# Kernel tuning notes

Hardware: AMD Instinct MI355X
Metric: run time of the kernel (lower is better)

The kernel has to match this reference:

```python
import jax, jax.numpy as jnp
import numpy as np

B, M, N, R, FIN, D, H = 16, 512, 512, 8, 4, 256, 4
DH = D // H
LGAT = 2
TF_RATE, THRESH = 0.9, 2.0
GAT_W, ORG_W, DET_W = 0.5, 0.5, 0.5


def setup_inputs() -> dict:
    key = jax.random.key(0)
    ks = jax.random.split(key, 16)
    g = lambda k, shp, fan: jax.random.normal(k, shp, jnp.float32) / np.sqrt(fan)
    inp = {
        'tracks': jax.random.normal(ks[0], (B, M, R, FIN), jnp.float32),
        'detections': jax.random.normal(ks[1], (B, N, FIN), jnp.float32),
        'tracklet_marks': jax.random.randint(ks[2], (B,), M // 2, M + 1, jnp.int32),
        'detection_marks': jax.random.randint(ks[3], (B,), N // 2, N + 1, jnp.int32),
        'feat_W1': g(ks[4], (FIN, D), FIN),
        'feat_b1': jnp.zeros((D,), jnp.float32),
        'feat_W2': g(ks[5], (D, D), D),
        'feat_b2': jnp.zeros((D,), jnp.float32),
        'enc_Wqkv': g(ks[6], (D, 3 * D), D),
        'enc_Wo': g(ks[7], (D, D), D),
        'enc_ff1': g(ks[8], (D, 4 * D), D),
        'enc_ff2': g(ks[9], (4 * D, D), 4 * D),
        'gat_W': g(ks[10], (LGAT, D, D), D),
        'gat_a': g(ks[11], (LGAT, 2, H, DH), DH),
        'det_gat_W': g(ks[12], (LGAT, D, D), D),
        'det_gat_a': g(ks[13], (LGAT, 2, H, DH), DH),
        'cls_Wq': g(ks[14], (2, D, D), D),
        'cls_Wk': g(ks[15], (2, D, D), D),
    }
    return inp


def _ln(x):
    m = jnp.mean(x, -1, keepdims=True)
    v = jnp.var(x, -1, keepdims=True)
    return (x - m) * jax.lax.rsqrt(v + 1e-5)


def _feat(x, W1, b1, W2, b2):
    return jax.nn.elu(x @ W1 + b1) @ W2 + b2


def _encoder(x, Wqkv, Wo, ff1, ff2):
    # x: [T, R, D] -> one pre-LN transformer layer over the rewind axis
    T = x.shape[0]
    h = _ln(x)
    qkv = (h @ Wqkv).reshape(T, R, 3, H, DH)
    q, k, v = qkv[:, :, 0], qkv[:, :, 1], qkv[:, :, 2]
    att = jax.nn.softmax(jnp.einsum('trhd,tshd->thrs', q, k) / np.sqrt(DH), axis=-1)
    o = jnp.einsum('thrs,tshd->trhd', att, v).reshape(T, R, D) @ Wo
    x = x + o
    return x + jax.nn.relu(_ln(x) @ ff1) @ ff2


def _gat(x, adj, W, a):
    # x: [B, Nn, D]; adj: [B, Nn, Nn] bool; a: [2, H, DH]
    b, nn_, _ = x.shape
    h = (x @ W).reshape(b, nn_, H, DH)
    src = jnp.einsum('bnhd,hd->bnh', h, a[0])
    dst = jnp.einsum('bnhd,hd->bnh', h, a[1])
    e = jax.nn.leaky_relu(src[:, :, None, :] + dst[:, None, :, :], 0.2)  # [B,Nn,Nn,H]
    e = jnp.where(adj[..., None], e, -1e9)
    alpha = jax.nn.softmax(e, axis=2)
    out = jnp.einsum('bijh,bjhd->bihd', alpha, h).reshape(b, nn_, D)
    return jax.nn.elu(out)


def _scores(x, adj_f, Wq, Wk):
    s = jax.nn.sigmoid(jnp.einsum('bid,bjd->bij', x @ Wq, x @ Wk) / np.sqrt(D))
    return s * adj_f


def _forward(tracks, detections, tracklet_marks, detection_marks,
             feat_W1, feat_b1, feat_W2, feat_b2,
             enc_Wqkv, enc_Wo, enc_ff1, enc_ff2,
             gat_W, gat_a, det_gat_W, det_gat_a, cls_Wq, cls_Wk):
    tr_emb = _feat(tracks, feat_W1, feat_b1, feat_W2, feat_b2)      # [B,M,R,D]
    det_emb = _feat(detections, feat_W1, feat_b1, feat_W2, feat_b2)  # [B,N,D]

    enc = _encoder(tr_emb.reshape(B * M, R, D), enc_Wqkv, enc_Wo, enc_ff1, enc_ff2)
    enc = enc.reshape(B, M, R, D)
    predicted = tr_emb[:, :, 0, :] + TF_RATE * enc[:, :, 0, :]       # [B,M,D]

    tmask = jnp.arange(M)[None, :] < tracklet_marks[:, None]
    dmask = jnp.arange(N)[None, :] < detection_marks[:, None]

    pos = jnp.concatenate([tracks[:, :, 0, :2], detections[:, :, :2]], axis=1)  # [B,M+N,2]
    vmask = jnp.concatenate([tmask, dmask], axis=1)
    dist = jnp.linalg.norm(pos[:, :, None, :] - pos[:, None, :, :], axis=-1)
    adj = (dist < THRESH) & vmask[:, :, None] & vmask[:, None, :]
    adj_f = adj.astype(jnp.float32)

    feat0 = jnp.concatenate([predicted, det_emb], axis=1)  # [B,M+N,D]
    x = feat0
    for l in range(LGAT):
        x = GAT_W * _gat(x, adj, gat_W[l], gat_a[l]) + ORG_W * feat0
    scores = _scores(x, adj_f, cls_Wq[0], cls_Wk[0])       # [B,M+N,M+N]
    asso_results = scores[:, :M, M:]                        # track->det block

    pd = detections[:, :, :2]
    dist_d = jnp.linalg.norm(pd[:, :, None, :] - pd[:, None, :, :], axis=-1)
    adj_d = (dist_d < THRESH) & dmask[:, :, None] & dmask[:, None, :]
    adj_d_f = adj_d.astype(jnp.float32)

    xd = det_emb
    for l in range(LGAT):
        xd = DET_W * _gat(xd, adj_d, det_gat_W[l], det_gat_a[l]) + ORG_W * det_emb
    det_scores = _scores(xd, adj_d_f, cls_Wq[1], cls_Wk[1])
    det_scores = det_scores * (1.0 - jnp.eye(N, dtype=jnp.float32))  # zero_diag

    return scores, det_scores, asso_results


def reference(tracks, detections, tracklet_marks, detection_marks,
              feat_W1, feat_b1, feat_W2, feat_b2,
              enc_Wqkv, enc_Wo, enc_ff1, enc_ff2,
              gat_W, gat_a, det_gat_W, det_gat_a, cls_Wq, cls_Wk):
    return _forward(tracks, detections, tracklet_marks, detection_marks,
                    feat_W1, feat_b1, feat_W2, feat_b2,
                    enc_Wqkv, enc_Wo, enc_ff1, enc_ff2,
                    gat_W, gat_a, det_gat_W, det_gat_a, cls_Wq, cls_Wk)
```

## Files before the change

### kernel.cpp

```cpp
#include <hip/hip_runtime.h>
#include <math.h>


typedef __bf16 bf16;
typedef __bf16 bf16x8 __attribute__((ext_vector_type(8)));
typedef __bf16 bf16x4 __attribute__((ext_vector_type(4)));
typedef float f32x4 __attribute__((ext_vector_type(4)));

__device__ __forceinline__ float bf2f(bf16 x) { return (float)x; }
__device__ __forceinline__ bf16 f2bf(float x) { return (bf16)x; }

__device__ __forceinline__ unsigned encf(float f) {
    unsigned u = __float_as_uint(f);
    return (u & 0x80000000u) ? ~u : (u | 0x80000000u);
}
__device__ __forceinline__ float decf(unsigned u) {
    return (u & 0x80000000u) ? __uint_as_float(u & 0x7fffffffu)
                             : __uint_as_float(~u);
}

struct PrepEnt { const float* src; long dofs; int R; int C; int tstart; int trans; };
struct PrepTab { PrepEnt e[13]; };

__global__ __launch_bounds__(256) void k_prep(PrepTab tab, bf16* __restrict__ dst)
{
    __shared__ float tile[32][33];
    const int tid = blockIdx.x;
    int k = 0;
    #pragma unroll
    for (int q = 1; q < 13; ++q) if (tid >= tab.e[q].tstart) k = q;
    PrepEnt E = tab.e[k];
    const int local = tid - E.tstart;
    const int cT = E.C >> 5;
    const int tr = local / cT, tc = local - tr * cT;
    const int r0 = tr << 5, c0 = tc << 5;
    const int t = threadIdx.x;
    {
        int r = t >> 3, cq = (t & 7) * 4;
        *(float4*)&tile[r][cq] = *(const float4*)(E.src + (long)(r0 + r) * E.C + c0 + cq);
    }
    __syncthreads();
    if (E.trans) {
        int c = t >> 3, rq = (t & 7) * 4;
        bf16x4 o;
        o[0] = f2bf(tile[rq + 0][c]); o[1] = f2bf(tile[rq + 1][c]);
        o[2] = f2bf(tile[rq + 2][c]); o[3] = f2bf(tile[rq + 3][c]);
        *(bf16x4*)(dst + E.dofs + (long)(c0 + c) * E.R + r0 + rq) = o;
    } else {
        int r = t >> 3, cq = (t & 7) * 4;
        bf16x4 o;
        o[0] = f2bf(tile[r][cq + 0]); o[1] = f2bf(tile[r][cq + 1]);
        o[2] = f2bf(tile[r][cq + 2]); o[3] = f2bf(tile[r][cq + 3]);
        *(bf16x4*)(dst + E.dofs + (long)(r0 + r) * E.C + c0 + cq) = o;
    }
}

__device__ __forceinline__ void gemm_bt_mn(const bf16* __restrict__ A, int lda,
                                           const bf16* __restrict__ BT, int ldb,
                                           int K, int m0, int n0, f32x4 acc[4])
{
    __shared__ bf16 As[64][40];
    __shared__ bf16 Bs[64][40];
    const int t = threadIdx.x;
    const int lane = t & 63, wv = t >> 6, lr = lane & 15, kq = lane >> 4;
    const int arow = t >> 2, acol = (t & 3) * 8;
    for (int k0 = 0; k0 < K; k0 += 32) {
        __syncthreads();
        *(uint4*)&As[arow][acol] = *(const uint4*)(A + (long)(m0 + arow) * lda + k0 + acol);
        *(uint4*)&Bs[arow][acol] = *(const uint4*)(BT + (long)(n0 + arow) * ldb + k0 + acol);
        __syncthreads();
        bf16x8 af = *(const bf16x8*)&As[wv * 16 + lr][kq * 8];
        #pragma unroll
        for (int nt = 0; nt < 4; ++nt) {
            bf16x8 bfr = *(const bf16x8*)&Bs[nt * 16 + lr][kq * 8];
            acc[nt] = __builtin_amdgcn_mfma_f32_16x16x32_bf16(af, bfr, acc[nt], 0, 0, 0);
        }
    }
}

__device__ __forceinline__ void gemm_bt(const bf16* __restrict__ A, int lda,
                                        const bf16* __restrict__ BT, int ldb,
                                        int K, f32x4 acc[4])
{
    gemm_bt_mn(A, lda, BT, ldb, K, blockIdx.y * 64, blockIdx.x * 64, acc);
}

__device__ __forceinline__ void gemm128_core(const bf16* __restrict__ A, int lda,
                                             const bf16* __restrict__ BT, int ldb,
                                             int m0, int n0, int K, f32x4 acc[2][8])
{
    __shared__ bf16 As[128][40];
    __shared__ bf16 Bs[128][40];
    const int t = threadIdx.x;
    const int lane = t & 63, wv = t >> 6, lr = lane & 15, kq = lane >> 4;
    const int srow = t >> 1, scol = (t & 1) * 16;
    for (int k0 = 0; k0 < K; k0 += 32) {
        __syncthreads();
        {
            const bf16* ap = A + (long)(m0 + srow) * lda + k0 + scol;
            *(uint4*)&As[srow][scol] = *(const uint4*)ap;
            *(uint4*)&As[srow][scol + 8] = *(const uint4*)(ap + 8);
            const bf16* bp = BT + (long)(n0 + srow) * ldb + k0 + scol;
            *(uint4*)&Bs[srow][scol] = *(const uint4*)bp;
            *(uint4*)&Bs[srow][scol + 8] = *(const uint4*)(bp + 8);
        }
        __syncthreads();
        bf16x8 af[2];
        af[0] = *(const bf16x8*)&As[wv * 32 + lr][kq * 8];
        af[1] = *(const bf16x8*)&As[wv * 32 + 16 + lr][kq * 8];
        #pragma unroll
        for (int nt = 0; nt < 8; ++nt) {
            bf16x8 bfr = *(const bf16x8*)&Bs[nt * 16 + lr][kq * 8];
            acc[0][nt] = __builtin_amdgcn_mfma_f32_16x16x32_bf16(af[0], bfr, acc[0][nt], 0, 0, 0);
            acc[1][nt] = __builtin_amdgcn_mfma_f32_16x16x32_bf16(af[1], bfr, acc[1][nt], 0, 0, 0);
        }
    }
}

__global__ __launch_bounds__(256) void k_gemm128_bf16(
    const bf16* __restrict__ A, int lda,
    const bf16* __restrict__ BT, int ldb,
    bf16* __restrict__ out, int ldo, int K, int relu)
{
    f32x4 acc[2][8] = {};
    const int m0 = blockIdx.y * 128, n0 = blockIdx.x * 128;
    gemm128_core(A, lda, BT, ldb, m0, n0, K, acc);
    const int lane = threadIdx.x & 63, wv = threadIdx.x >> 6;
    const int lr = lane & 15, kq = lane >> 4;
    #pragma unroll
    for (int mt = 0; mt < 2; ++mt) {
        #pragma unroll
        for (int nt = 0; nt < 8; ++nt) {
            int col = n0 + nt * 16 + lr;
            #pragma unroll
            for (int i = 0; i < 4; ++i) {
                int row = m0 + wv * 32 + mt * 16 + kq * 4 + i;
                float v = acc[mt][nt][i];
                if (relu) v = fmaxf(v, 0.f);
                out[(long)row * ldo + col] = f2bf(v);
            }
        }
    }
}

__global__ __launch_bounds__(256) void k_kvq(
    const bf16* __restrict__ hln, const bf16* __restrict__ WqkvT,
    bf16* __restrict__ kv, bf16* __restrict__ q)
{
    const int wg = (blockIdx.x & 7) * 272 + (blockIdx.x >> 3);
    const bf16* A; const bf16* BT; bf16* out;
    int lda, ldo, m0, n0;
    if (wg < 2048) {
        A = hln; lda = 256; BT = WqkvT + 65536;
        m0 = (wg >> 2) * 128; n0 = (wg & 3) * 128;
        out = kv; ldo = 512;
    } else {
        int t2 = wg - 2048;
        A = hln; lda = 2048; BT = WqkvT;
        m0 = (t2 >> 1) * 128; n0 = (t2 & 1) * 128;
        out = q; ldo = 256;
    }
    f32x4 acc[2][8] = {};
    gemm128_core(A, lda, BT, 256, m0, n0, 256, acc);
    const int lane = threadIdx.x & 63, wv = threadIdx.x >> 6;
    const int lr = lane & 15, kq = lane >> 4;
    #pragma unroll
    for (int mt = 0; mt < 2; ++mt) {
        #pragma unroll
        for (int nt = 0; nt < 8; ++nt) {
            int col = n0 + nt * 16 + lr;
            #pragma unroll
            for (int i = 0; i < 4; ++i) {
                int row = m0 + wv * 32 + mt * 16 + kq * 4 + i;
                out[(long)row * ldo + col] = f2bf(acc[mt][nt][i]);
            }
        }
    }
}

__global__ __launch_bounds__(256) void k_wcomb(bf16* __restrict__ wb)
{
    const int bid = blockIdx.x;
    const int head = bid >> 4, r = bid & 15;
    const bf16* A  = wb + 1179648 + head * 131072;
    const bf16* BT = wb + 1114112 + head * 131072;
    bf16* out = wb + 1376256 + head * 65536;
    const int m0 = (r >> 2) * 64, n0 = (r & 3) * 64;
    f32x4 acc[4] = {};
    gemm_bt_mn(A, 256, BT, 256, 256, m0, n0, acc);
    const int lane = threadIdx.x & 63, wv = threadIdx.x >> 6;
    const int lr = lane & 15, kq = lane >> 4;
    #pragma unroll
    for (int nt = 0; nt < 4; ++nt) {
        int col = n0 + nt * 16 + lr;
        #pragma unroll
        for (int i = 0; i < 4; ++i) {
            int row = m0 + wv * 16 + kq * 4 + i;
            out[(long)row * 256 + col] = f2bf(acc[nt][i]);
        }
    }
}

__global__ __launch_bounds__(256) void k_y(
    const bf16* __restrict__ xm, const bf16* __restrict__ WcT0, bf16* __restrict__ ym,
    const bf16* __restrict__ xd, const bf16* __restrict__ WcT1, bf16* __restrict__ yd)
{
    const int wg = (blockIdx.x & 7) * 192 + (blockIdx.x >> 3);
    int by = wg >> 2;
    const int bx = wg & 3;
    const bf16 *A, *BT; bf16* out;
    if (by < 256) { A = xm; BT = WcT0; out = ym; }
    else          { by -= 256; A = xd; BT = WcT1; out = yd; }
    f32x4 acc[4] = {};
    const int m0 = by * 64, n0 = bx * 64;
    gemm_bt_mn(A, 256, BT, 256, 256, m0, n0, acc);
    const int lane = threadIdx.x & 63, wv = threadIdx.x >> 6;
    const int lr = lane & 15, kq = lane >> 4;
    #pragma unroll
    for (int nt = 0; nt < 4; ++nt) {
        int col = n0 + nt * 16 + lr;
        #pragma unroll
        for (int i = 0; i < 4; ++i) {
            int row = m0 + wv * 16 + kq * 4 + i;
            out[(long)row * 256 + col] = f2bf(acc[nt][i]);
        }
    }
}

__global__ __launch_bounds__(256) void k_logits(
    const bf16* __restrict__ ym, const bf16* __restrict__ xm,
    const bf16* __restrict__ yd, const bf16* __restrict__ xd,
    const unsigned long long* __restrict__ adjmM,
    const unsigned long long* __restrict__ adjmD,
    float* __restrict__ out, float* __restrict__ asso)
{
    const int wg = (blockIdx.x & 7) * 160 + (blockIdx.x >> 3);
    const bf16 *A, *BT; float* ob; const unsigned long long* adjm;
    int ldo, nN, nC, flags, m0, n0, z;
    if (wg < 1024) {
        z = wg >> 6; int r = wg & 63;
        m0 = (r >> 3) * 128; n0 = (r & 7) * 128;
        A = ym + (long)z * 262144; BT = xm + (long)z * 262144;
        ob = out + (long)z * 1048576; ldo = 1024;
        adjm = adjmM; nN = 1024; nC = 16; flags = 1;
    } else {
        int t2 = wg - 1024;
        z = t2 >> 4; int r = t2 & 15;
        m0 = (r >> 2) * 128; n0 = (r & 3) * 128;
        A = yd + (long)z * 131072; BT = xd + (long)z * 131072;
        ob = out + 16777216 + (long)z * 262144; ldo = 512;
        adjm = adjmD; nN = 512; nC = 8; flags = 2;
    }
    const int t = threadIdx.x;
    const int lane = t & 63, wv = t >> 6, lr = lane & 15, kq = lane >> 4;
    f32x4 acc[2][8] = {};
    {
        __shared__ bf16 As[128][72];
        __shared__ bf16 Bs[128][72];
        const int srow4 = t >> 3, scol8 = (t & 7) * 8;
        for (int k0 = 0; k0 < 256; k0 += 64) {
            __syncthreads();
            #pragma unroll
            for (int p = 0; p < 4; ++p) {
                int row = p * 32 + srow4;
                *(uint4*)&As[row][scol8] = *(const uint4*)(A + (long)(m0 + row) * 256 + k0 + scol8);
                *(uint4*)&Bs[row][scol8] = *(const uint4*)(BT + (long)(n0 + row) * 256 + k0 + scol8);
            }
            __syncthreads();
            #pragma unroll
            for (int ks = 0; ks < 64; ks += 32) {
                bf16x8 af[2];
                af[0] = *(const bf16x8*)&As[wv * 32 + lr][kq * 8 + ks];
                af[1] = *(const bf16x8*)&As[wv * 32 + 16 + lr][kq * 8 + ks];
                #pragma unroll
                for (int nt = 0; nt < 8; ++nt) {
                    bf16x8 bfr = *(const bf16x8*)&Bs[nt * 16 + lr][kq * 8 + ks];
                    acc[0][nt] = __builtin_amdgcn_mfma_f32_16x16x32_bf16(af[0], bfr, acc[0][nt], 0, 0, 0);
                    acc[1][nt] = __builtin_amdgcn_mfma_f32_16x16x32_bf16(af[1], bfr, acc[1][nt], 0, 0, 0);
                }
            }
        }
    }
    #pragma unroll
    for (int mt = 0; mt < 2; ++mt) {
        #pragma unroll
        for (int i = 0; i < 4; ++i) {
            int row = m0 + wv * 32 + mt * 16 + kq * 4 + i;
            unsigned long long w0 = adjm[((long)z * nN + row) * nC + (n0 >> 6)];
            unsigned long long w1 = adjm[((long)z * nN + row) * nC + (n0 >> 6) + 1];
            #pragma unroll
            for (int nt = 0; nt < 8; ++nt) {
                int col = n0 + nt * 16 + lr;
                int bp = nt * 16 + lr;
                bool adj = (bp < 64) ? ((w0 >> bp) & 1ull) : ((w1 >> (bp - 64)) & 1ull);
                if ((flags & 2) && row == col) adj = false;
                float v = 0.f;
                if (adj) v = 1.f / (1.f + __expf(-acc[mt][nt][i] * 0.0625f));
                ob[(long)row * ldo + col] = v;
                if ((flags & 1) && row < 512 && col >= 512)
                    asso[(long)z * 262144 + (long)row * 512 + (col - 512)] = v;
            }
        }
    }
}

__global__ __launch_bounds__(256) void k_gemm_pred(
    const bf16* __restrict__ A, int lda,
    const bf16* __restrict__ BT, int ldb,
    const float* __restrict__ res1, const float* __restrict__ res2,
    float* __restrict__ outf, bf16* __restrict__ outb, int K)
{
    f32x4 acc[4] = {};
    gemm_bt(A, lda, BT, ldb, K, acc);
    const int lane = threadIdx.x & 63, wv = threadIdx.x >> 6;
    const int lr = lane & 15, kq = lane >> 4;
    const int m0 = blockIdx.y * 64, n0 = blockIdx.x * 64;
    #pragma unroll
    for (int nt = 0; nt < 4; ++nt) {
        int col = n0 + nt * 16 + lr;
        #pragma unroll
        for (int i = 0; i < 4; ++i) {
            int row = m0 + wv * 16 + kq * 4 + i;
            float v = res1[(long)row * 256 + col]
                    + 0.9f * (res2[(long)row * 256 + col] + acc[nt][i]);
            long drow = (long)row + ((row >> 9) << 9);
            long o = drow * 256 + col;
            outf[o] = v;
            outb[o] = f2bf(v);
        }
    }
}

__global__ __launch_bounds__(256) void k_featgemm(
    const float* __restrict__ tracks, const float* __restrict__ dets,
    const float* __restrict__ W1, const float* __restrict__ b1,
    const bf16* __restrict__ W2T, const float* __restrict__ b2,
    bf16* __restrict__ hln, float* __restrict__ emb_r0_f,
    float* __restrict__ feat0_f, bf16* __restrict__ feat0_b,
    bf16* __restrict__ demb_b)
{
    __shared__ float xr[64][4];
    __shared__ float w1s[4][256];
    __shared__ float b1s[256];
    __shared__ bf16 As[64][40];
    __shared__ bf16 Bs[256][40];
    const int t = threadIdx.x;
    const int m0 = blockIdx.x * 64;
    if (t < 64) {
        int gr = m0 + t;
        const float* sp = (gr < 65536) ? (tracks + (long)gr * 4)
                                       : (dets + (long)(gr - 65536) * 4);
        *(float4*)&xr[t][0] = *(const float4*)sp;
    }
    w1s[0][t] = W1[t];       w1s[1][t] = W1[256 + t];
    w1s[2][t] = W1[512 + t]; w1s[3][t] = W1[768 + t];
    b1s[t] = b1[t];
    const int arow = t >> 2, acol = (t & 3) * 8;
    const int lane = t & 63, wv = t >> 6, lr = lane & 15, kq = lane >> 4;
    f32x4 acc[16] = {};
    __syncthreads();
    for (int k0 = 0; k0 < 256; k0 += 32) {
        __syncthreads();
        #pragma unroll
        for (int j = 0; j < 8; ++j) {
            int c = k0 + acol + j;
            float v = fmaf(xr[arow][0], w1s[0][c],
                      fmaf(xr[arow][1], w1s[1][c],
                      fmaf(xr[arow][2], w1s[2][c],
                      fmaf(xr[arow][3], w1s[3][c], b1s[c]))));
            v = v > 0.f ? v : (__expf(v) - 1.f);
            As[arow][acol + j] = f2bf(v);
        }
        #pragma unroll
        for (int rr = 0; rr < 4; ++rr) {
            int n = rr * 64 + (t >> 2);
            *(uint4*)&Bs[n][acol] = *(const uint4*)(W2T + (long)n * 256 + k0 + acol);
        }
        __syncthreads();
        bf16x8 af = *(const bf16x8*)&As[wv * 16 + lr][kq * 8];
        #pragma unroll
        for (int nt = 0; nt < 16; ++nt) {
            bf16x8 bfr = *(const bf16x8*)&Bs[nt * 16 + lr][kq * 8];
            acc[nt] = __builtin_amdgcn_mfma_f32_16x16x32_bf16(af, bfr, acc[nt], 0, 0, 0);
        }
    }
    if (m0 < 65536) {
        #pragma unroll
        for (int nt = 0; nt < 16; ++nt) {
            int col = nt * 16 + lr;
            float bv = b2[col];
            #pragma unroll
            for (int i = 0; i < 4; ++i) {
                int gr = m0 + wv * 16 + kq * 4 + i;
                float v = acc[nt][i] + bv;
                if ((gr & 7) == 0) emb_r0_f[(long)(gr >> 3) * 256 + col] = v;
                acc[nt][i] = bf2f(f2bf(v));
            }
        }
        float mean[4], rstd[4];
        #pragma unroll
        for (int i = 0; i < 4; ++i) {
            float s1 = 0.f, s2 = 0.f;
            #pragma unroll
            for (int nt = 0; nt < 16; ++nt) {
                float v = acc[nt][i];
                s1 += v; s2 += v * v;
            }
            #pragma unroll
            for (int o = 1; o < 16; o <<= 1) {
                s1 += __shfl_xor(s1, o, 64);
                s2 += __shfl_xor(s2, o, 64);
            }
            float mu = s1 * (1.f / 256.f);
            mean[i] = mu;
            rstd[i] = rsqrtf(fmaxf(s2 * (1.f / 256.f) - mu * mu, 0.f) + 1e-5f);
        }
        #pragma unroll
        for (int nt = 0; nt < 16; ++nt) {
            int col = nt * 16 + lr;
            #pragma unroll
            for (int i = 0; i < 4; ++i) {
                int gr = m0 + wv * 16 + kq * 4 + i;
                hln[(long)gr * 256 + col] = f2bf((acc[nt][i] - mean[i]) * rstd[i]);
            }
        }
    } else {
        #pragma unroll
        for (int nt = 0; nt < 16; ++nt) {
            int col = nt * 16 + lr;
            float bv = b2[col];
            #pragma unroll
            for (int i = 0; i < 4; ++i) {
                int gr = m0 + wv * 16 + kq * 4 + i;
                float v = acc[nt][i] + bv;
                int dr = gr - 65536;
                long drow = ((long)(dr >> 9) << 10) + 512 + (dr & 511);
                feat0_f[drow * 256 + col] = v;
                feat0_b[drow * 256 + col] = f2bf(v);
                demb_b[(long)dr * 256 + col] = f2bf(v);
            }
        }
    }
}

__global__ __launch_bounds__(256) void k_adjmask(
    const float4* __restrict__ nodes,
    unsigned long long* __restrict__ adjm_main,
    unsigned long long* __restrict__ adjm_det)
{
    __shared__ float4 nds[1024];
    int bid = blockIdx.x;
    int nN, b, i0, nodeOfs;
    unsigned long long* adjm;
    if (bid < 512) { nN = 1024; b = bid >> 5; i0 = (bid & 31) << 5; nodeOfs = 0; adjm = adjm_main; }
    else { int b2 = bid - 512; nN = 512; b = b2 >> 4; i0 = (b2 & 15) << 5; nodeOfs = 512; adjm = adjm_det; }
    const float4* nb = nodes + b * 1024 + nodeOfs;
    const int t = threadIdx.x;
    for (int j = t; j < nN; j += 256) nds[j] = nb[j];
    __syncthreads();
    const int w = t >> 6, l = t & 63;
    const int nC = nN >> 6;
    for (int ii = 0; ii < 8; ++ii) {
        int i = i0 + w * 8 + ii;
        float4 ni = nds[i];
        for (int c = 0; c < nC; ++c) {
            float4 nj = nds[c * 64 + l];
            float dx = ni.x - nj.x, dy = ni.y - nj.y;
            bool adj = (dx * dx + dy * dy < 4.f) && (ni.z + nj.z < 1.f);
            unsigned long long mask = __ballot(adj);
            if (l == 0) adjm[(long)(b * nN + i) * nC + c] = mask;
        }
    }
}

__global__ __launch_bounds__(256) void k_addres_ln(
    const bf16* __restrict__ A, const bf16* __restrict__ BT,
    const float* __restrict__ res1,
    float* __restrict__ x2out, bf16* __restrict__ h2)
{
    __shared__ bf16 As[64][40];
    __shared__ bf16 Bs[256][40];
    const int t = threadIdx.x;
    const int m0 = blockIdx.x * 64;
    const int arow = t >> 2, acol = (t & 3) * 8;
    const int lane = t & 63, wv = t >> 6, lr = lane & 15, kq = lane >> 4;
    f32x4 acc[16] = {};
    for (int k0 = 0; k0 < 256; k0 += 32) {
        __syncthreads();
        *(uint4*)&As[arow][acol] = *(const uint4*)(A + (long)(m0 + arow) * 256 + k0 + acol);
        #pragma unroll
        for (int rr = 0; rr < 4; ++rr) {
            int n = rr * 64 + (t >> 2);
            *(uint4*)&Bs[n][acol] = *(const uint4*)(BT + (long)n * 256 + k0 + acol);
        }
        __syncthreads();
        bf16x8 af = *(const bf16x8*)&As[wv * 16 + lr][kq * 8];
        #pragma unroll
        for (int nt = 0; nt < 16; ++nt) {
            bf16x8 bfr = *(const bf16x8*)&Bs[nt * 16 + lr][kq * 8];
            acc[nt] = __builtin_amdgcn_mfma_f32_16x16x32_bf16(af, bfr, acc[nt], 0, 0, 0);
        }
    }
    float mean[4], rstd[4];
    #pragma unroll
    for (int i = 0; i < 4; ++i) {
        int row = m0 + wv * 16 + kq * 4 + i;
        float s1 = 0.f, s2 = 0.f;
        #pragma unroll
        for (int nt = 0; nt < 16; ++nt) {
            float v = res1[(long)row * 256 + nt * 16 + lr] + acc[nt][i];
            acc[nt][i] = v;
            s1 += v; s2 += v * v;
        }
        #pragma unroll
        for (int o = 1; o < 16; o <<= 1) {
            s1 += __shfl_xor(s1, o, 64);
            s2 += __shfl_xor(s2, o, 64);
        }
        float mu = s1 * (1.f / 256.f);
        mean[i] = mu;
        rstd[i] = rsqrtf(fmaxf(s2 * (1.f / 256.f) - mu * mu, 0.f) + 1e-5f);
    }
    #pragma unroll
    for (int nt = 0; nt < 16; ++nt) {
        int col = nt * 16 + lr;
        #pragma unroll
        for (int i = 0; i < 4; ++i) {
            int row = m0 + wv * 16 + kq * 4 + i;
            float v = acc[nt][i];
            x2out[(long)row * 256 + col] = v;
            h2[(long)row * 256 + col] = f2bf((v - mean[i]) * rstd[i]);
        }
    }
}

__global__ __launch_bounds__(256) void k_attn(
    const bf16* __restrict__ q, const bf16* __restrict__ kv,
    bf16* __restrict__ o0)
{
    const long t = blockIdx.x;
    const int h = threadIdx.x >> 6;
    const int lane = threadIdx.x & 63;
    const int s = lane >> 3;
    const int dg = lane & 7;
    const bf16* qp = q + t * 256 + h * 64 + dg * 8;
    const bf16* kp = kv + (t * 8 + s) * 512 + h * 64 + dg * 8;
    float p = 0.f;
    #pragma unroll
    for (int e = 0; e < 8; ++e) p += bf2f(qp[e]) * bf2f(kp[e]);
    p += __shfl_xor(p, 1, 64);
    p += __shfl_xor(p, 2, 64);
    p += __shfl_xor(p, 4, 64);
    float sc = p * 0.125f;
    float w[8];
    float mx = -1e30f;
    #pragma unroll
    for (int s2 = 0; s2 < 8; ++s2) { w[s2] = __shfl(sc, s2 * 8, 64); mx = fmaxf(mx, w[s2]); }
    float sum = 0.f;
    #pragma unroll
    for (int s2 = 0; s2 < 8; ++s2) { w[s2] = __expf(w[s2] - mx); sum += w[s2]; }
    float rs = 1.f / sum;
    float acc = 0.f;
    const bf16* vp = kv + (t * 8) * 512 + 256 + h * 64 + lane;
    #pragma unroll
    for (int s2 = 0; s2 < 8; ++s2) acc += w[s2] * bf2f(vp[(long)s2 * 512]);
    o0[t * 256 + h * 64 + lane] = f2bf(acc * rs);
}

__global__ __launch_bounds__(256) void k_nodes(
    const float* __restrict__ tracks, const float* __restrict__ dets,
    const int* __restrict__ tm, const int* __restrict__ dm,
    float4* __restrict__ nodes, unsigned* __restrict__ maxd_all)
{
    int idx = blockIdx.x * 256 + threadIdx.x;
    if (blockIdx.x == 0) maxd_all[threadIdx.x] = 0x007fffffu;
    int b = idx >> 10;
    int i = idx & 1023;
    float x, y;
    int valid;
    if (i < 512) {
        long o = (long)(b * 512 + i) * 32;
        x = tracks[o]; y = tracks[o + 1];
        valid = (i < tm[b]) ? 1 : 0;
    } else {
        int n = i - 512;
        long o = (long)(b * 512 + n) * 4;
        x = dets[o]; y = dets[o + 1];
        valid = (n < dm[b]) ? 1 : 0;
    }
    nodes[idx] = make_float4(x, y, valid ? 0.f : 1e9f, 0.f);
}

__global__ __launch_bounds__(256) void k_gemmT_src(
    const bf16* __restrict__ WTm, const bf16* __restrict__ Xm, bf16* __restrict__ hgTm,
    const float* __restrict__ avm, float* __restrict__ srcm, float* __restrict__ dstm,
    unsigned* __restrict__ mxm,
    const bf16* __restrict__ WTd, const bf16* __restrict__ Xd, bf16* __restrict__ hgTd,
    const float* __restrict__ avd, float* __restrict__ srcd, float* __restrict__ dstd,
    unsigned* __restrict__ mxd)
{
    __shared__ float sred[4][2][64];
    const int wg = (blockIdx.x & 7) * 192 + (blockIdx.x >> 3);
    const int h = wg & 3;
    int bx = wg >> 2;
    const bf16 *WT, *X; bf16* hgT; const float* av;
    float *src, *dst; unsigned* mx; int nN, nLog;
    if (bx < 256) { WT = WTm; X = Xm; hgT = hgTm; av = avm; src = srcm; dst = dstm; mx = mxm; nN = 1024; nLog = 10; }
    else { bx -= 256; WT = WTd; X = Xd; hgT = hgTd; av = avd; src = srcd; dst = dstd; mx = mxd; nN = 512; nLog = 9; }
    const int d0 = h * 64, n0 = bx * 64;
    f32x4 acc[4] = {};
    gemm_bt_mn(WT, 256, X, 256, 256, d0, n0, acc);
    const int t = threadIdx.x, lane = t & 63, wv = t >> 6, lr = lane & 15, kq = lane >> 4;
    float a0c[4], a1c[4];
    *(float4*)a0c = *(const float4*)(av + h * 64 + wv * 16 + kq * 4);
    *(float4*)a1c = *(const float4*)(av + 256 + h * 64 + wv * 16 + kq * 4);
    #pragma unroll
    for (int nt = 0; nt < 4; ++nt) {
        int node = n0 + nt * 16 + lr;
        int b = node >> nLog;
        int j = node & (nN - 1);
        float p0 = 0.f, p1 = 0.f;
        #pragma unroll
        for (int i = 0; i < 4; ++i) {
            int d = d0 + wv * 16 + kq * 4 + i;
            bf16 vb = f2bf(acc[nt][i]);
            hgT[((long)(b * 256 + d) << nLog) + j] = vb;
            float vr = bf2f(vb);
            p0 += vr * a0c[i];
            p1 += vr * a1c[i];
        }
        p0 += __shfl_xor(p0, 16, 64); p0 += __shfl_xor(p0, 32, 64);
        p1 += __shfl_xor(p1, 16, 64); p1 += __shfl_xor(p1, 32, 64);
        if (kq == 0) { sred[wv][0][nt * 16 + lr] = p0; sred[wv][1][nt * 16 + lr] = p1; }
    }
    __syncthreads();
    if (t < 64) {
        float s0 = sred[0][0][t] + sred[1][0][t] + sred[2][0][t] + sred[3][0][t];
        float s1 = sred[0][1][t] + sred[1][1][t] + sred[2][1][t] + sred[3][1][t];
        int node = n0 + t;
        src[(long)node * 4 + h] = s0;
        dst[(long)node * 4 + h] = s1;
        float m = s1;
        #pragma unroll
        for (int o = 32; o; o >>= 1) m = fmaxf(m, __shfl_xor(m, o, 64));
        if (t == 0) atomicMax(&mx[(n0 >> nLog) * 4 + h], encf(m));
    }
}

__global__ __launch_bounds__(256) void k_gatagg2(
    const bf16* __restrict__ hgTm, const unsigned long long* __restrict__ adjmM,
    const float4* __restrict__ srcM, const unsigned* __restrict__ mxM,
    const float4* __restrict__ dstM, const float* __restrict__ resM, bf16* __restrict__ outM,
    const bf16* __restrict__ hgTd, const unsigned long long* __restrict__ adjmD,
    const float4* __restrict__ srcD, const unsigned* __restrict__ mxD,
    const float4* __restrict__ dstD, const float* __restrict__ resD, bf16* __restrict__ outD)
{
    __shared__ float dstT[4][1024];
    __shared__ unsigned int adjW[32][33];
    int bid = (blockIdx.x & 7) * 96 + (blockIdx.x >> 3);
    const bf16* hgT; const unsigned long long* adjm; const float4* srcv;
    const unsigned* mxp; const float4* dstv; const float* res; bf16* outb; int nN;
    if (bid < 512) { hgT = hgTm; adjm = adjmM; srcv = srcM; mxp = mxM; dstv = dstM; res = resM; outb = outM; nN = 1024; }
    else { bid -= 512; hgT = hgTd; adjm = adjmD; srcv = srcD; mxp = mxD; dstv = dstD; res = resD; outb = outD; nN = 512; }
    const int t = threadIdx.x;
    const int nblk = nN >> 5;
    const int b = bid / nblk;
    const int i0 = (bid - b * nblk) << 5;
    const int nC = nN >> 6;
    for (int j = t; j < nN; j += 256) {
        float4 dj = dstv[(long)b * nN + j];
        dstT[0][j] = dj.x; dstT[1][j] = dj.y; dstT[2][j] = dj.z; dstT[3][j] = dj.w;
    }
    for (int idx = t; idx < 32 * nC; idx += 256) {
        int r = idx / nC, c = idx - r * nC;
        unsigned long long v = adjm[((long)b * nN + i0 + r) * nC + c];
        adjW[r][c * 2] = (unsigned)v;
        adjW[r][c * 2 + 1] = (unsigned)(v >> 32);
    }
    __syncthreads();
    const int h = t >> 6, lane = t & 63, lr = lane & 15, kq = lane >> 4;
    const float mdh = decf(mxp[b * 4 + h]);
    float s_r[2], m_r[2], psum[2] = {0.f, 0.f};
    #pragma unroll
    for (int mt = 0; mt < 2; ++mt) {
        long idx = (long)b * nN + i0 + mt * 16 + lr;
        s_r[mt] = ((const float*)(srcv + idx))[h];
        float tmp = s_r[mt] + mdh;
        m_r[mt] = fmaxf(tmp, 0.2f * tmp);
    }
    f32x4 acc[2][4] = {};
    const bf16* hb = hgT + ((long)b * 256 + h * 64) * nN;
    for (int j0 = 0; j0 < nN; j0 += 32) {
        bf16x8 bfr[4];
        #pragma unroll
        for (int nt = 0; nt < 4; ++nt)
            bfr[nt] = *(const bf16x8*)(hb + (long)(nt * 16 + lr) * nN + j0 + kq * 8);
        #pragma unroll
        for (int mt = 0; mt < 2; ++mt) {
            unsigned byte = (adjW[mt * 16 + lr][j0 >> 5] >> (kq * 8)) & 0xffu;
            bf16x8 af;
            float ps = 0.f;
            #pragma unroll
            for (int jj = 0; jj < 8; ++jj) {
                float e = s_r[mt] + dstT[h][j0 + kq * 8 + jj];
                e = fmaxf(e, 0.2f * e);
                e = (byte & (1u << jj)) ? e : -1e9f;
                float p = __expf(e - m_r[mt]);
                af[jj] = f2bf(p);
                ps += p;
            }
            psum[mt] += ps;
            #pragma unroll
            for (int nt = 0; nt < 4; ++nt)
                acc[mt][nt] = __builtin_amdgcn_mfma_f32_16x16x32_bf16(af, bfr[nt], acc[mt][nt], 0, 0, 0);
        }
    }
    float stot[2];
    #pragma unroll
    for (int mt = 0; mt < 2; ++mt) {
        float v = psum[mt];
        v += __shfl_xor(v, 16, 64);
        v += __shfl_xor(v, 32, 64);
        stot[mt] = v;
    }
    #pragma unroll
    for (int mt = 0; mt < 2; ++mt) {
        #pragma unroll
        for (int ii = 0; ii < 4; ++ii) {
            int i = i0 + mt * 16 + kq * 4 + ii;
            long bi = (long)b * nN + i;
            float sv = __shfl(stot[mt], kq * 4 + ii, 64);
            float rs = 1.f / fmaxf(sv, 1e-30f);
            #pragma unroll
            for (int nt = 0; nt < 4; ++nt) {
                int col = h * 64 + nt * 16 + lr;
                float a = acc[mt][nt][ii] * rs;
                float e = a > 0.f ? a : expm1f(a);
                float v = 0.5f * e + 0.5f * res[(long)b * 262144 + (long)i * 256 + col];
                outb[bi * 256 + col] = f2bf(v);
            }
        }
    }
}

extern "C" void kernel_launch(void* const* d_in, const int* in_sizes, int n_in,
                              void* d_out, int out_size, void* d_ws, size_t ws_size,
                              hipStream_t stream)
{
    (void)in_sizes; (void)n_in; (void)out_size; (void)ws_size;
    const float* tracks = (const float*)d_in[0];
    const float* dets   = (const float*)d_in[1];
    const int*  tmarks = (const int*)d_in[2];
    const int*  dmarks = (const int*)d_in[3];
    const float* W1   = (const float*)d_in[4];
    const float* b1   = (const float*)d_in[5];
    const float* W2   = (const float*)d_in[6];
    const float* b2   = (const float*)d_in[7];
    const float* Wqkv = (const float*)d_in[8];
    const float* Wo   = (const float*)d_in[9];
    const float* eff1 = (const float*)d_in[10];
    const float* eff2 = (const float*)d_in[11];
    const float* gatW = (const float*)d_in[12];
    const float* gatA = (const float*)d_in[13];
    const float* dgatW = (const float*)d_in[14];
    const float* dgatA = (const float*)d_in[15];
    const float* clsWq = (const float*)d_in[16];
    const float* clsWk = (const float*)d_in[17];
    float* out = (float*)d_out;

    char* wsb = (char*)d_ws;
    size_t off = 0;
    auto take = [&](size_t bytes) -> char* {
        char* p = wsb + off;
        off += (bytes + 255) & ~(size_t)255;
        return p;
    };
    char* R_emb  = take(37748736);
    char* R_r0   = take(8388608);
    char* R_hln  = take(33554432);
    char* R_v    = take(33554432);
    char* R_gat  = take(25165824);
    char* R_q    = take(4194304);
    char* R_o0   = take(4194304);
    char* R_f0f  = take(16777216);
    char* R_f0b  = take(8388608);
    char* R_demb = take(4194304);
    float4* nodes = (float4*)take(262144);
    float4* src4  = (float4*)take(262144);
    float4* dst4  = (float4*)take(262144);
    unsigned* maxd_all = (unsigned*)take(1024);
    unsigned long long* adjm_main = (unsigned long long*)take(2097152);
    unsigned long long* adjm_det  = (unsigned long long*)take(524288);
    bf16* wbuf = (bf16*)take(3014656);
    float4* srcd4 = (float4*)take(131072);
    float4* dstd4 = (float4*)take(131072);

    float* emb_r0_f = (float*)R_r0;
    bf16*  hln      = (bf16*)R_hln;
    bf16*  kv_b     = (bf16*)d_out;
    bf16*  q_b      = (bf16*)R_q;
    bf16*  o0_b     = (bf16*)R_o0;
    float* x20      = (float*)R_emb;
    bf16*  h2_b     = (bf16*)(R_emb + 8388608);
    bf16*  f1_b     = (bf16*)R_hln;
    float* feat0_f  = (float*)R_f0f;
    bf16*  feat0_b  = (bf16*)R_f0b;
    bf16*  demb_b   = (bf16*)R_demb;
    bf16*  hgT_m    = (bf16*)R_gat;
    bf16*  xga_m    = (bf16*)(R_gat + 8388608);
    bf16*  xgb_m    = (bf16*)(R_gat + 16777216);
    bf16*  hgT_d    = (bf16*)(R_emb + 16777216);
    bf16*  xga_d    = (bf16*)(R_emb + 20971520);
    bf16*  xgb_d    = (bf16*)(R_emb + 25165824);
    bf16*  y_m      = (bf16*)R_v;
    bf16*  y_d      = (bf16*)(R_v + 8388608);

    bf16* W2T    = wbuf + 0;
    bf16* WqkvT  = wbuf + 65536;
    bf16* WoT    = wbuf + 262144;
    bf16* eff1T  = wbuf + 327680;
    bf16* eff2T  = wbuf + 589824;
    bf16* gatW0T = wbuf + 851968;
    bf16* gatW1T = wbuf + 917504;
    bf16* dgatW0T= wbuf + 983040;
    bf16* dgatW1T= wbuf + 1048576;
    bf16* WcT0   = wbuf + 1376256;
    bf16* WcT1   = wbuf + 1441792;
    PrepTab tab;
    tab.e[0]  = { W2,             0,       256,  256,  0,    1 };
    tab.e[1]  = { Wqkv,           65536,   256,  768,  64,   1 };
    tab.e[2]  = { Wo,             262144,  256,  256,  256,  1 };
    tab.e[3]  = { eff1,           327680,  256,  1024, 320,  1 };
    tab.e[4]  = { eff2,           589824,  1024, 256,  576,  1 };
    tab.e[5]  = { gatW,           851968,  256,  256,  832,  1 };
    tab.e[6]  = { gatW + 65536,   917504,  256,  256,  896,  1 };
    tab.e[7]  = { dgatW,          983040,  256,  256,  960,  1 };
    tab.e[8]  = { dgatW + 65536,  1048576, 256,  256,  1024, 1 };
    tab.e[9]  = { clsWq,          1114112, 256,  256,  1088, 0 };
    tab.e[10] = { clsWk,          1179648, 256,  256,  1152, 0 };
    tab.e[11] = { clsWq + 65536,  1245184, 256,  256,  1216, 0 };
    tab.e[12] = { clsWk + 65536,  1310720, 256,  256,  1280, 0 };

    k_prep<<<1344, 256, 0, stream>>>(tab, wbuf);
    k_wcomb<<<32, 256, 0, stream>>>(wbuf);
    k_nodes<<<64, 256, 0, stream>>>(tracks, dets, tmarks, dmarks, nodes, maxd_all);
    k_adjmask<<<768, 256, 0, stream>>>(nodes, adjm_main, adjm_det);
    k_featgemm<<<1152, 256, 0, stream>>>(tracks, dets, W1, b1, W2T, b2,
        hln, emb_r0_f, feat0_f, feat0_b, demb_b);

    k_kvq<<<2176, 256, 0, stream>>>(hln, WqkvT, kv_b, q_b);
    k_attn<<<8192, 256, 0, stream>>>(q_b, kv_b, o0_b);
    k_addres_ln<<<128, 256, 0, stream>>>(o0_b, WoT, emb_r0_f, x20, h2_b);
    k_gemm128_bf16<<<dim3(8, 64, 1), 256, 0, stream>>>(h2_b, 256, eff1T, 256, f1_b, 1024, 256, 1);
    k_gemm_pred<<<dim3(4, 128, 1), 256, 0, stream>>>(f1_b, 1024, eff2T, 1024, emb_r0_f, x20, feat0_f, feat0_b, 1024);

    k_gemmT_src<<<1536, 256, 0, stream>>>(
        gatW0T, feat0_b, hgT_m, gatA, (float*)src4, (float*)dst4, maxd_all,
        dgatW0T, demb_b, hgT_d, dgatA, (float*)srcd4, (float*)dstd4, maxd_all + 128);
    k_gatagg2<<<768, 256, 0, stream>>>(
        hgT_m, adjm_main, src4, maxd_all, dst4, feat0_f, xga_m,
        hgT_d, adjm_det, srcd4, maxd_all + 128, dstd4, feat0_f + 131072, xga_d);
    k_gemmT_src<<<1536, 256, 0, stream>>>(
        gatW1T, xga_m, hgT_m, gatA + 512, (float*)src4, (float*)dst4, maxd_all + 64,
        dgatW1T, xga_d, hgT_d, dgatA + 512, (float*)srcd4, (float*)dstd4, maxd_all + 192);
    k_gatagg2<<<768, 256, 0, stream>>>(
        hgT_m, adjm_main, src4, maxd_all + 64, dst4, feat0_f, xgb_m,
        hgT_d, adjm_det, srcd4, maxd_all + 192, dstd4, feat0_f + 131072, xgb_d);

    k_y<<<1536, 256, 0, stream>>>(xgb_m, WcT0, y_m, xgb_d, WcT1, y_d);
    k_logits<<<1280, 256, 0, stream>>>(y_m, xgb_m, y_d, xgb_d, adjm_main, adjm_det,
        out, out + 20971520L);
}
```

Before: 497.2 us.

## Halve GAT aggregation row tile and fold softmax into exp2 with precomputed offsets

Each GAT aggregation block now covers 16 destination rows instead of 32, which doubles the grid to 1536 blocks for more parallelism. The softmax exponent is restructured: scores are pre-scaled by log2(e) in shared memory, the leaky-relu minus max is rewritten as max(u+d, 0.2d+w) and evaluated with exp2f, and masked entries become zero after the exp rather than via a -1e9 sentinel. dstT reads are vectorised as float4. The cost is that each B fragment (hgT) is now reused for only one M tile instead of two, so global and L2 traffic for the feature matrix roughly doubles.

```diff
diff --git a/kernel.cpp b/kernel.cpp
--- a/kernel.cpp
+++ b/kernel.cpp
@@ -655,23 +655,25 @@
     const float4* __restrict__ srcD, const unsigned* __restrict__ mxD,
     const float4* __restrict__ dstD, const float* __restrict__ resD, bf16* __restrict__ outD)
 {
+    const float L2E = 1.44269504f;
     __shared__ float dstT[4][1024];
-    __shared__ unsigned int adjW[32][33];
-    int bid = (blockIdx.x & 7) * 96 + (blockIdx.x >> 3);
+    __shared__ unsigned adjW[16][33];
+    int bid = (blockIdx.x & 7) * 192 + (blockIdx.x >> 3);
     const bf16* hgT; const unsigned long long* adjm; const float4* srcv;
     const unsigned* mxp; const float4* dstv; const float* res; bf16* outb; int nN;
-    if (bid < 512) { hgT = hgTm; adjm = adjmM; srcv = srcM; mxp = mxM; dstv = dstM; res = resM; outb = outM; nN = 1024; }
-    else { bid -= 512; hgT = hgTd; adjm = adjmD; srcv = srcD; mxp = mxD; dstv = dstD; res = resD; outb = outD; nN = 512; }
+    if (bid < 1024) { hgT = hgTm; adjm = adjmM; srcv = srcM; mxp = mxM; dstv = dstM; res = resM; outb = outM; nN = 1024; }
+    else { bid -= 1024; hgT = hgTd; adjm = adjmD; srcv = srcD; mxp = mxD; dstv = dstD; res = resD; outb = outD; nN = 512; }
     const int t = threadIdx.x;
-    const int nblk = nN >> 5;
+    const int nblk = nN >> 4;
     const int b = bid / nblk;
-    const int i0 = (bid - b * nblk) << 5;
+    const int i0 = (bid - b * nblk) << 4;
     const int nC = nN >> 6;
     for (int j = t; j < nN; j += 256) {
         float4 dj = dstv[(long)b * nN + j];
-        dstT[0][j] = dj.x; dstT[1][j] = dj.y; dstT[2][j] = dj.z; dstT[3][j] = dj.w;
-    }
-    for (int idx = t; idx < 32 * nC; idx += 256) {
+        dstT[0][j] = dj.x * L2E; dstT[1][j] = dj.y * L2E;
+        dstT[2][j] = dj.z * L2E; dstT[3][j] = dj.w * L2E;
+    }
+    for (int idx = t; idx < 16 * nC; idx += 256) {
         int r = idx / nC, c = idx - r * nC;
         unsigned long long v = adjm[((long)b * nN + i0 + r) * nC + c];
         adjW[r][c * 2] = (unsigned)v;
@@ -679,66 +681,54 @@
     }
     __syncthreads();
     const int h = t >> 6, lane = t & 63, lr = lane & 15, kq = lane >> 4;
-    const float mdh = decf(mxp[b * 4 + h]);
-    float s_r[2], m_r[2], psum[2] = {0.f, 0.f};
-    #pragma unroll
-    for (int mt = 0; mt < 2; ++mt) {
-        long idx = (long)b * nN + i0 + mt * 16 + lr;
-        s_r[mt] = ((const float*)(srcv + idx))[h];
-        float tmp = s_r[mt] + mdh;
-        m_r[mt] = fmaxf(tmp, 0.2f * tmp);
-    }
-    f32x4 acc[2][4] = {};
+    const float mdh = decf(mxp[b * 4 + h]) * L2E;
+    float s_r = ((const float*)(srcv + (long)b * nN + i0 + lr))[h] * L2E;
+    float tmp = s_r + mdh;
+    float m_r = fmaxf(tmp, 0.2f * tmp);
+    float u = s_r - m_r;
+    float w = fmaf(0.2f, s_r, -m_r);
+    float psum = 0.f;
+    f32x4 acc[4] = {};
     const bf16* hb = hgT + ((long)b * 256 + h * 64) * nN;
     for (int j0 = 0; j0 < nN; j0 += 32) {
         bf16x8 bfr[4];
         #pragma unroll
         for (int nt = 0; nt < 4; ++nt)
             bfr[nt] = *(const bf16x8*)(hb + (long)(nt * 16 + lr) * nN + j0 + kq * 8);
-        #pragma unroll
-        for (int mt = 0; mt < 2; ++mt) {
-            unsigned byte = (adjW[mt * 16 + lr][j0 >> 5] >> (kq * 8)) & 0xffu;
-            bf16x8 af;
-            float ps = 0.f;
-            #pragma unroll
-            for (int jj = 0; jj < 8; ++jj) {
-                float e = s_r[mt] + dstT[h][j0 + kq * 8 + jj];
-                e = fmaxf(e, 0.2f * e);
-                e = (byte & (1u << jj)) ? e : -1e9f;
-                float p = __expf(e - m_r[mt]);
-                af[jj] = f2bf(p);
-                ps += p;
-            }
-            psum[mt] += ps;
-            #pragma unroll
-            for (int nt = 0; nt < 4; ++nt)
-                acc[mt][nt] = __builtin_amdgcn_mfma_f32_16x16x32_bf16(af, bfr[nt], acc[mt][nt], 0, 0, 0);
-        }
-    }
-    float stot[2];
-    #pragma unroll
-    for (int mt = 0; mt < 2; ++mt) {
-        float v = psum[mt];
-        v += __shfl_xor(v, 16, 64);
-        v += __shfl_xor(v, 32, 64);
-        stot[mt] = v;
-    }
-    #pragma unroll
-    for (int mt = 0; mt < 2; ++mt) {
-        #pragma unroll
-        for (int ii = 0; ii < 4; ++ii) {
-            int i = i0 + mt * 16 + kq * 4 + ii;
-            long bi = (long)b * nN + i;
-            float sv = __shfl(stot[mt], kq * 4 + ii, 64);
-            float rs = 1.f / fmaxf(sv, 1e-30f);
-            #pragma unroll
-            for (int nt = 0; nt < 4; ++nt) {
-                int col = h * 64 + nt * 16 + lr;
-                float a = acc[mt][nt][ii] * rs;
-                float e = a > 0.f ? a : expm1f(a);
-                float v = 0.5f * e + 0.5f * res[(long)b * 262144 + (long)i * 256 + col];
-                outb[bi * 256 + col] = f2bf(v);
-            }
+        unsigned byte = (adjW[lr][j0 >> 5] >> (kq * 8)) & 0xffu;
+        float4 d0 = *(const float4*)&dstT[h][j0 + kq * 8];
+        float4 d1 = *(const float4*)&dstT[h][j0 + kq * 8 + 4];
+        float dv[8] = {d0.x, d0.y, d0.z, d0.w, d1.x, d1.y, d1.z, d1.w};
+        bf16x8 af;
+        #pragma unroll
+        for (int jj = 0; jj < 8; ++jj) {
+            float x = fmaxf(u + dv[jj], fmaf(0.2f, dv[jj], w));
+            float p = exp2f(x);
+            p = (byte & (1u << jj)) ? p : 0.f;
+            af[jj] = f2bf(p);
+            psum += p;
+        }
+        #pragma unroll
+        for (int nt = 0; nt < 4; ++nt)
+            acc[nt] = __builtin_amdgcn_mfma_f32_16x16x32_bf16(af, bfr[nt], acc[nt], 0, 0, 0);
+    }
+    float v = psum;
+    v += __shfl_xor(v, 16, 64);
+    v += __shfl_xor(v, 32, 64);
+    float stot = v;
+    #pragma unroll
+    for (int ii = 0; ii < 4; ++ii) {
+        int i = i0 + kq * 4 + ii;
+        long bi = (long)b * nN + i;
+        float sv = __shfl(stot, kq * 4 + ii, 64);
+        float rs = 1.f / fmaxf(sv, 1e-30f);
+        #pragma unroll
+        for (int nt = 0; nt < 4; ++nt) {
+            int col = h * 64 + nt * 16 + lr;
+            float a = acc[nt][ii] * rs;
+            float e = a > 0.f ? a : expm1f(a);
+            float vv = 0.5f * e + 0.5f * res[(long)b * 262144 + (long)i * 256 + col];
+            outb[bi * 256 + col] = f2bf(vv);
         }
     }
 }
@@ -857,13 +847,13 @@
     k_gemmT_src<<<1536, 256, 0, stream>>>(
         gatW0T, feat0_b, hgT_m, gatA, (float*)src4, (float*)dst4, maxd_all,
         dgatW0T, demb_b, hgT_d, dgatA, (float*)srcd4, (float*)dstd4, maxd_all + 128);
-    k_gatagg2<<<768, 256, 0, stream>>>(
+    k_gatagg2<<<1536, 256, 0, stream>>>(
         hgT_m, adjm_main, src4, maxd_all, dst4, feat0_f, xga_m,
         hgT_d, adjm_det, srcd4, maxd_all + 128, dstd4, feat0_f + 131072, xga_d);
     k_gemmT_src<<<1536, 256, 0, stream>>>(
         gatW1T, xga_m, hgT_m, gatA + 512, (float*)src4, (float*)dst4, maxd_all + 64,
         dgatW1T, xga_d, hgT_d, dgatA + 512, (float*)srcd4, (float*)dstd4, maxd_all + 192);
-    k_gatagg2<<<768, 256, 0, stream>>>(
+    k_gatagg2<<<1536, 256, 0, stream>>>(
         hgT_m, adjm_main, src4, maxd_all + 64, dst4, feat0_f, xgb_m,
         hgT_d, adjm_det, srcd4, maxd_all + 192, dstd4, feat0_f + 131072, xgb_d);
 
```

Result: slower. 563.3 us (+13.3%).

## Remap GAT aggregation blocks to one head per block with exp2-folded softmax

Applied to the files above, without the earlier changes.

Reworks the GAT aggregation kernel so each block handles a single head over 128 rows, with each wave covering 32 rows, where before a block covered all four heads over 32 rows. Only that head's destination scores are staged, and they are read back as vector loads. The softmax exponent is rewritten in base 2 with the log2(e) factor and the row max folded into precomputed per-row terms. Masked entries are now set to zero after the exponent instead of being pushed to -1e9 before it. Adjacency staging grows to 128 rows per block. Neighbouring blocks no longer share the same rows across heads, which changes how the feature matrix and outputs are reused in cache.

```diff
diff --git a/kernel.cpp b/kernel.cpp
--- a/kernel.cpp
+++ b/kernel.cpp
@@ -647,7 +647,7 @@
     }
 }
 
-__global__ __launch_bounds__(256) void k_gatagg2(
+__global__ __launch_bounds__(256) void k_gatagg3(
     const bf16* __restrict__ hgTm, const unsigned long long* __restrict__ adjmM,
     const float4* __restrict__ srcM, const unsigned* __restrict__ mxM,
     const float4* __restrict__ dstM, const float* __restrict__ resM, bf16* __restrict__ outM,
@@ -655,38 +655,46 @@
     const float4* __restrict__ srcD, const unsigned* __restrict__ mxD,
     const float4* __restrict__ dstD, const float* __restrict__ resD, bf16* __restrict__ outD)
 {
-    __shared__ float dstT[4][1024];
-    __shared__ unsigned int adjW[32][33];
+    const float L2E = 1.44269504f;
+    __shared__ float dstT[1024];
+    __shared__ unsigned adjW[128][33];
     int bid = (blockIdx.x & 7) * 96 + (blockIdx.x >> 3);
     const bf16* hgT; const unsigned long long* adjm; const float4* srcv;
-    const unsigned* mxp; const float4* dstv; const float* res; bf16* outb; int nN;
-    if (bid < 512) { hgT = hgTm; adjm = adjmM; srcv = srcM; mxp = mxM; dstv = dstM; res = resM; outb = outM; nN = 1024; }
-    else { bid -= 512; hgT = hgTd; adjm = adjmD; srcv = srcD; mxp = mxD; dstv = dstD; res = resD; outb = outD; nN = 512; }
+    const unsigned* mxp; const float4* dstv; const float* res; bf16* outb;
+    int nN, b, h, i0;
+    if (bid < 512) {
+        hgT = hgTm; adjm = adjmM; srcv = srcM; mxp = mxM; dstv = dstM; res = resM; outb = outM;
+        nN = 1024; b = bid >> 5; int r = bid & 31; h = r >> 3; i0 = (r & 7) << 7;
+    } else {
+        int b2 = bid - 512;
+        hgT = hgTd; adjm = adjmD; srcv = srcD; mxp = mxD; dstv = dstD; res = resD; outb = outD;
+        nN = 512; b = b2 >> 4; int r = b2 & 15; h = r >> 2; i0 = (r & 3) << 7;
+    }
     const int t = threadIdx.x;
-    const int nblk = nN >> 5;
-    const int b = bid / nblk;
-    const int i0 = (bid - b * nblk) << 5;
-    const int nC = nN >> 6;
-    for (int j = t; j < nN; j += 256) {
-        float4 dj = dstv[(long)b * nN + j];
-        dstT[0][j] = dj.x; dstT[1][j] = dj.y; dstT[2][j] = dj.z; dstT[3][j] = dj.w;
-    }
-    for (int idx = t; idx < 32 * nC; idx += 256) {
-        int r = idx / nC, c = idx - r * nC;
-        unsigned long long v = adjm[((long)b * nN + i0 + r) * nC + c];
-        adjW[r][c * 2] = (unsigned)v;
-        adjW[r][c * 2 + 1] = (unsigned)(v >> 32);
+    const int nW = nN >> 5;
+    const int sh = (nN == 1024) ? 5 : 4;
+    for (int j = t; j < nN; j += 256)
+        dstT[j] = ((const float*)(dstv + (long)b * nN + j))[h] * L2E;
+    {
+        const unsigned* adj32 = (const unsigned*)(adjm + (long)(b * nN + i0) * (nN >> 6));
+        for (int idx = t; idx < (nW << 7); idx += 256) {
+            int r = idx >> sh, c = idx & (nW - 1);
+            adjW[r][c] = adj32[(long)r * nW + c];
+        }
     }
     __syncthreads();
-    const int h = t >> 6, lane = t & 63, lr = lane & 15, kq = lane >> 4;
-    const float mdh = decf(mxp[b * 4 + h]);
-    float s_r[2], m_r[2], psum[2] = {0.f, 0.f};
+    const int lane = t & 63, wv = t >> 6, lr = lane & 15, kq = lane >> 4;
+    const int ri = i0 + wv * 32;
+    const float mdh = decf(mxp[b * 4 + h]) * L2E;
+    float u[2], w[2], psum[2] = {0.f, 0.f};
     #pragma unroll
     for (int mt = 0; mt < 2; ++mt) {
-        long idx = (long)b * nN + i0 + mt * 16 + lr;
-        s_r[mt] = ((const float*)(srcv + idx))[h];
-        float tmp = s_r[mt] + mdh;
-        m_r[mt] = fmaxf(tmp, 0.2f * tmp);
+        int row = ri + mt * 16 + lr;
+        float s = ((const float*)(srcv + (long)b * nN + row))[h] * L2E;
+        float tmp = s + mdh;
+        float m = fmaxf(tmp, 0.2f * tmp);
+        u[mt] = s - m;
+        w[mt] = fmaf(0.2f, s, -m);
     }
     f32x4 acc[2][4] = {};
     const bf16* hb = hgT + ((long)b * 256 + h * 64) * nN;
@@ -695,17 +703,19 @@
         #pragma unroll
         for (int nt = 0; nt < 4; ++nt)
             bfr[nt] = *(const bf16x8*)(hb + (long)(nt * 16 + lr) * nN + j0 + kq * 8);
+        float4 d0 = *(const float4*)&dstT[j0 + kq * 8];
+        float4 d1 = *(const float4*)&dstT[j0 + kq * 8 + 4];
+        float dv[8] = {d0.x, d0.y, d0.z, d0.w, d1.x, d1.y, d1.z, d1.w};
         #pragma unroll
         for (int mt = 0; mt < 2; ++mt) {
-            unsigned byte = (adjW[mt * 16 + lr][j0 >> 5] >> (kq * 8)) & 0xffu;
+            unsigned byte = (adjW[wv * 32 + mt * 16 + lr][j0 >> 5] >> (kq * 8)) & 0xffu;
             bf16x8 af;
             float ps = 0.f;
             #pragma unroll
             for (int jj = 0; jj < 8; ++jj) {
-                float e = s_r[mt] + dstT[h][j0 + kq * 8 + jj];
-                e = fmaxf(e, 0.2f * e);
-                e = (byte & (1u << jj)) ? e : -1e9f;
-                float p = __expf(e - m_r[mt]);
+                float x = fmaxf(u[mt] + dv[jj], fmaf(0.2f, dv[jj], w[mt]));
+                float p = exp2f(x);
+                p = (byte & (1u << jj)) ? p : 0.f;
                 af[jj] = f2bf(p);
                 ps += p;
             }
@@ -727,7 +737,7 @@
     for (int mt = 0; mt < 2; ++mt) {
         #pragma unroll
         for (int ii = 0; ii < 4; ++ii) {
-            int i = i0 + mt * 16 + kq * 4 + ii;
+            int i = ri + mt * 16 + kq * 4 + ii;
             long bi = (long)b * nN + i;
             float sv = __shfl(stot[mt], kq * 4 + ii, 64);
             float rs = 1.f / fmaxf(sv, 1e-30f);
@@ -736,8 +746,8 @@
                 int col = h * 64 + nt * 16 + lr;
                 float a = acc[mt][nt][ii] * rs;
                 float e = a > 0.f ? a : expm1f(a);
-                float v = 0.5f * e + 0.5f * res[(long)b * 262144 + (long)i * 256 + col];
-                outb[bi * 256 + col] = f2bf(v);
+                float vv = 0.5f * e + 0.5f * res[(long)b * 262144 + (long)i * 256 + col];
+                outb[bi * 256 + col] = f2bf(vv);
             }
         }
     }
@@ -857,13 +867,13 @@
     k_gemmT_src<<<1536, 256, 0, stream>>>(
         gatW0T, feat0_b, hgT_m, gatA, (float*)src4, (float*)dst4, maxd_all,
         dgatW0T, demb_b, hgT_d, dgatA, (float*)srcd4, (float*)dstd4, maxd_all + 128);
-    k_gatagg2<<<768, 256, 0, stream>>>(
+    k_gatagg3<<<768, 256, 0, stream>>>(
         hgT_m, adjm_main, src4, maxd_all, dst4, feat0_f, xga_m,
         hgT_d, adjm_det, srcd4, maxd_all + 128, dstd4, feat0_f + 131072, xga_d);
     k_gemmT_src<<<1536, 256, 0, stream>>>(
         gatW1T, xga_m, hgT_m, gatA + 512, (float*)src4, (float*)dst4, maxd_all + 64,
         dgatW1T, xga_d, hgT_d, dgatA + 512, (float*)srcd4, (float*)dstd4, maxd_all + 192);
-    k_gatagg2<<<768, 256, 0, stream>>>(
+    k_gatagg3<<<768, 256, 0, stream>>>(
         hgT_m, adjm_main, src4, maxd_all + 64, dst4, feat0_f, xgb_m,
         hgT_d, adjm_det, srcd4, maxd_all + 192, dstd4, feat0_f + 131072, xgb_d);
 
```

New measurement: 494.1 us. Within noise of the previous version (-0.6%).
